# Kernel optimization log

Hardware: AMD Instinct MI355X
Metric: run time of the kernel (lower is better)

## Reference

```python
import jax, jax.numpy as jnp
import numpy as np

B, D, LP, P = 64, 256, 64, 16
N = 256                     # linear1 output = number of graph nodes (= d_model for consistent reassembly)
F = LP * P                  # per-node feature dim = SAGEConv input_dim = 1024
HID = 512                   # hidden_channels
NODE_SLICES = {"A": (0, 128), "B": (128, 192), "C": (192, 256)}
# 6 cross edge types + 3 self-loop edge types (add_self_loops=True)
EDGE_TYPES = [("A", "B"), ("B", "A"), ("A", "C"), ("C", "A"), ("B", "C"), ("C", "B"),
              ("A", "A"), ("B", "B"), ("C", "C")]
E = len(EDGE_TYPES)


def setup_inputs() -> dict:
    ks = jax.random.split(jax.random.key(0), 8)
    s = lambda fan: 1.0 / np.sqrt(fan)
    return {
        "x": jax.random.normal(ks[0], (B, D, LP, P), jnp.float32),
        "W1": jax.random.normal(ks[1], (D, N), jnp.float32) * s(D),   # linear1
        "b1": jnp.zeros((N,), jnp.float32),
        "Wl": jax.random.normal(ks[2], (E, F, HID), jnp.float32) * s(F),  # SAGEConv lin_l (aggregated msgs)
        "bl": jnp.zeros((E, HID), jnp.float32),
        "Wr": jax.random.normal(ks[3], (E, F, HID), jnp.float32) * s(F),  # SAGEConv lin_r (root, no bias)
        "Wf": jax.random.normal(ks[4], (HID, F), jnp.float32) * s(HID),   # final_linear
        "bf": jnp.zeros((F,), jnp.float32),
        "W2": jax.random.normal(ks[5], (N, D), jnp.float32) * s(N),       # linear2
        "b2": jnp.zeros((D,), jnp.float32),
        "period": P,
    }


def reference(x, W1, b1, Wl, bl, Wr, Wf, bf, W2, b2, period):
    b = x.shape[0]
    # linear1 over channel dim: [B,D,LP,P] -> [B,N,LP,P]
    h = jnp.einsum('bdlp,dn->bnlp', x, W1) + b1[None, :, None, None]
    hf = h.reshape(b, N, -1)                                  # node features [B, N, F]
    xt = {t: hf[:, lo:hi] for t, (lo, hi) in NODE_SLICES.items()}
    # complete bipartite graph => scatter-mean over incoming edges == mean over all src nodes
    mu = {t: v.mean(axis=1) for t, v in xt.items()}           # [B, F]
    contribs = {t: [] for t in NODE_SLICES}
    for i, (s_t, d_t) in enumerate(EDGE_TYPES):
        # SAGEConv(mean): lin_l(aggr msgs) + lin_r(x_dst)
        c = (mu[s_t] @ Wl[i] + bl[i])[:, None, :] + jnp.einsum('bnf,fh->bnh', xt[d_t], Wr[i])
        contribs[d_t].append(c)
    outs = []
    for t in ("A", "B", "C"):
        o = jnp.mean(jnp.stack(contribs[t]), axis=0)          # HeteroConv aggr='mean' over edge types
        o = jax.nn.relu(o) @ Wf + bf                          # relu + final_linear -> [B, n_t, F]
        outs.append(o)
    out = jnp.concatenate(outs, axis=1)                       # [B, N, F] (A,B,C slices are contiguous)
    out = out.reshape(b, N, -1, period)                       # [B, N, LP, P]
    # linear2 over node/channel dim
    y = jnp.einsum('bnlp,nd->bdlp', out, W2) + b2[None, :, None, None]
    return y
```

## Files before the change

### kernel.cpp

```cpp
#include <hip/hip_runtime.h>

typedef unsigned short u16;
typedef __attribute__((ext_vector_type(8))) short bf16x8;
typedef __attribute__((ext_vector_type(4))) float f32x4;

constexpr int BB = 64;
constexpr int NN = 256;
constexpr int SS = 1024;
constexpr int FF = 1024;
constexpr int HH = 512;

__device__ const int d_eArr[3][3] = {{1, 3, 6}, {0, 5, 7}, {2, 4, 8}};
__device__ const int d_slotE[3][3] = {{2, 0, 0}, {0, 2, 1}, {1, 1, 2}};

__device__ __forceinline__ u16 f2bf(float f) {
    union { float f; unsigned u; } v; v.f = f;
    unsigned r = v.u + 0x7FFFu + ((v.u >> 16) & 1u);
    return (u16)(r >> 16);
}
__device__ __forceinline__ float bf2f(u16 h) {
    union { unsigned u; float f; } v; v.u = ((unsigned)h) << 16;
    return v.f;
}

typedef const __attribute__((address_space(1))) void gv_t;
typedef __attribute__((address_space(3))) void lv_t;
__device__ __forceinline__ void gl16(const void* g, void* l) {
    __builtin_amdgcn_global_load_lds((gv_t*)g, (lv_t*)l, 16, 0, 0);
}
__device__ __forceinline__ int swzv(int r) { return (r ^ (r >> 2)) & 3; }

template<int N> __device__ __forceinline__ void waitvm();
template<> __device__ __forceinline__ void waitvm<0>()  { asm volatile("s_waitcnt vmcnt(0)" ::: "memory"); }
template<> __device__ __forceinline__ void waitvm<2>()  { asm volatile("s_waitcnt vmcnt(2)" ::: "memory"); }
template<> __device__ __forceinline__ void waitvm<4>()  { asm volatile("s_waitcnt vmcnt(4)" ::: "memory"); }
template<> __device__ __forceinline__ void waitvm<6>()  { asm volatile("s_waitcnt vmcnt(6)" ::: "memory"); }
template<> __device__ __forceinline__ void waitvm<8>()  { asm volatile("s_waitcnt vmcnt(8)" ::: "memory"); }
template<> __device__ __forceinline__ void waitvm<12>() { asm volatile("s_waitcnt vmcnt(12)" ::: "memory"); }

__device__ __forceinline__ int g5row(int t, int g, int r) {
    if (t == 0) return (g << 8) + r;
    const int bp = (t == 1) ? (g - 64) : (g - 96);
    const int b  = (bp << 1) + (r >> 6);
    const int n  = ((t == 1) ? 128 : 192) + (r & 63);
    return (b << 8) + n;
}

__global__ __launch_bounds__(256)
void transpose_bf16(const float* __restrict__ in, u16* __restrict__ out, int R, int C) {
    __shared__ float tile[32][33];
    const int b = blockIdx.z;
    in  += (size_t)b * R * C;
    out += (size_t)b * R * C;
    const int c0 = blockIdx.x * 32, r0 = blockIdx.y * 32;
    const int x = threadIdx.x & 31, y = threadIdx.x >> 5;
#pragma unroll
    for (int k = 0; k < 4; ++k)
        tile[y + 8 * k][x] = in[(size_t)(r0 + y + 8 * k) * C + c0 + x];
    __syncthreads();
#pragma unroll
    for (int k = 0; k < 4; ++k)
        out[(size_t)(c0 + y + 8 * k) * R + r0 + x] = f2bf(tile[x][y + 8 * k]);
}

__device__ __forceinline__ void tr32(const float* __restrict__ in, u16* __restrict__ out,
                                     int R, int C, int bx, int by, float (*tile)[33]) {
    const int c0 = bx * 32, r0 = by * 32;
    const int x = threadIdx.x & 31, y = threadIdx.x >> 5;
#pragma unroll
    for (int k = 0; k < 4; ++k)
        tile[y + 8 * k][x] = in[(size_t)(r0 + y + 8 * k) * C + c0 + x];
    __syncthreads();
#pragma unroll
    for (int k = 0; k < 4; ++k)
        out[(size_t)(c0 + y + 8 * k) * R + r0 + x] = f2bf(tile[x][y + 8 * k]);
}

__global__ __launch_bounds__(256)
void prep_weights(const float* __restrict__ W1, const float* __restrict__ W2,
                  const float* __restrict__ Wf, const float* __restrict__ Wl,
                  const float* __restrict__ Wr, const float* __restrict__ bl,
                  u16* __restrict__ W1T, u16* __restrict__ W2T, u16* __restrict__ WfT,
                  u16* __restrict__ WlTc, u16* __restrict__ WsumT, float* __restrict__ blsum)
{
    __shared__ float tile[32][33];
    int id = blockIdx.x;
    if (id < 64) { tr32(W1, W1T, 256, 256, id & 7, id >> 3, tile); return; }
    id -= 64;
    if (id < 64) { tr32(W2, W2T, 256, 256, id & 7, id >> 3, tile); return; }
    id -= 64;
    if (id < 512) { tr32(Wf, WfT, 512, 1024, id & 31, id >> 5, tile); return; }
    id -= 512;
    if (id < 4608) {
        const int p = id >> 9, rem = id & 511;
        const int bx = rem & 15, by = rem >> 4;
        const int t = p / 3, ep = p % 3, e = d_eArr[t][ep];
        const int h0 = bx * 32, f0 = by * 32;
        const int x = threadIdx.x & 31, y = threadIdx.x >> 5;
        const float* src = Wl + (size_t)e * FF * HH;
#pragma unroll
        for (int k = 0; k < 4; ++k)
            tile[y + 8 * k][x] = src[(size_t)(f0 + y + 8 * k) * HH + h0 + x];
        __syncthreads();
        u16* dst = WlTc + (size_t)t * HH * 3072 + (size_t)ep * 1024;
#pragma unroll
        for (int k = 0; k < 4; ++k)
            dst[(size_t)(h0 + y + 8 * k) * 3072 + f0 + x] = f2bf(tile[x][y + 8 * k]);
        return;
    }
    id -= 4608;
    if (id < 1536) {
        const int t = id >> 9, rem = id & 511;
        const int bx = rem & 15, by = rem >> 4;
        const int h0 = bx * 32, f0 = by * 32;
        const int x = threadIdx.x & 31, y = threadIdx.x >> 5;
        const int e0 = d_eArr[t][0], e1 = d_eArr[t][1], e2 = d_eArr[t][2];
#pragma unroll
        for (int k = 0; k < 4; ++k) {
            const size_t off = (size_t)(f0 + y + 8 * k) * HH + h0 + x;
            float s = Wr[(size_t)e0 * FF * HH + off] + Wr[(size_t)e1 * FF * HH + off] +
                      Wr[(size_t)e2 * FF * HH + off];
            tile[y + 8 * k][x] = s * (1.f / 3.f);
        }
        __syncthreads();
        u16* dst = WsumT + (size_t)t * HH * FF;
#pragma unroll
        for (int k = 0; k < 4; ++k)
            dst[(size_t)(h0 + y + 8 * k) * FF + f0 + x] = f2bf(tile[x][y + 8 * k]);
        return;
    }
#pragma unroll
    for (int j = 0; j < 6; ++j) {
        const int idx = j * 256 + threadIdx.x;
        const int t = idx >> 9, hh = idx & 511;
        blsum[t * HH + hh] = bl[d_eArr[t][0] * HH + hh] + bl[d_eArr[t][1] * HH + hh] +
                             bl[d_eArr[t][2] * HH + hh];
    }
}

template<int BM, int BN, int KLEN, int EPI, int MODE>
__global__ __launch_bounds__(256, 2)
void gemm2(const u16* __restrict__ Abase, const u16* __restrict__ Bbase,
           void* __restrict__ Cbase, const float* __restrict__ aux1,
           const float* __restrict__ aux2, u16* __restrict__ muOut,
           long long sB, long long sC, int ldA, int ldB, int ldC)
{
    constexpr int WM = BM / 2, WN = BN / 2;
    constexpr int FM = WM / 16, FN = WN / 16;
    constexpr int NIA = (BM * 4) / 256, NIB = (BN * 4) / 256;
    constexpr int LPS = NIA + NIB;
    constexpr int BUFB = (BM + BN) * 64;
    constexpr int NT = KLEN / 32;
    static_assert(NT >= 3, "need >=3 K-steps");
    __shared__ __align__(16) unsigned char smem[3 * BUFB];

    const int tid = threadIdx.x, lane = tid & 63, wave = tid >> 6;
    const int wm = wave >> 1, wn = wave & 1;
    const int n0 = blockIdx.x * BN;

    int m0 = 0, b = 0, t = 0, g = 0;
    const u16* Ab; const u16* Bb;
    if constexpr (MODE == 0) {
        b  = blockIdx.z;
        m0 = blockIdx.y * BM;
        Ab = Abase + (size_t)m0 * ldA;
        Bb = Bbase + (size_t)b * sB + (size_t)n0 * ldB;
    } else if constexpr (MODE == 1) {
        g  = blockIdx.y;
        t  = (g < 64) ? 0 : (g < 96 ? 1 : 2);
        Ab = Abase;
        Bb = Bbase + (size_t)t * (HH * FF) + (size_t)n0 * ldB;
    } else {
        t  = blockIdx.z;
        const int k0 = blockIdx.y * KLEN;
        Ab = Abase + (size_t)t * 64 * ldA + k0;
        Bb = Bbase + (size_t)t * (HH * 3072) + (size_t)n0 * ldB + k0;
    }

    const u16* gAp[NIA]; const u16* gBp[NIB];
    int lAo[NIA], lBo[NIB];
#pragma unroll
    for (int i = 0; i < NIA; ++i) {
        const int c = i * 256 + tid, r = c >> 2, jl = c & 3;
        const int js = jl ^ swzv(r);
        size_t rowoff;
        if constexpr (MODE == 1) rowoff = (size_t)g5row(t, g, r) * FF;
        else                     rowoff = (size_t)r * ldA;
        gAp[i] = Ab + rowoff + js * 8;
        lAo[i] = c * 16;
    }
#pragma unroll
    for (int i = 0; i < NIB; ++i) {
        const int c = i * 256 + tid, r = c >> 2, jl = c & 3;
        const int js = jl ^ swzv(r);
        gBp[i] = Bb + (size_t)r * ldB + js * 8;
        lBo[i] = BM * 64 + c * 16;
    }
    const int q = lane >> 4;
    int rAo[FM], rBo[FN];
#pragma unroll
    for (int i = 0; i < FM; ++i) {
        const int r = wm * WM + i * 16 + (lane & 15);
        rAo[i] = (r * 4 + (q ^ swzv(r))) * 16;
    }
#pragma unroll
    for (int j = 0; j < FN; ++j) {
        const int r = wn * WN + j * 16 + (lane & 15);
        rBo[j] = BM * 64 + (r * 4 + (q ^ swzv(r))) * 16;
    }

    char* sm = (char*)smem;
    auto stage = [&](int bufo, int it) {
        const int kofs = it * 32;
#pragma unroll
        for (int i = 0; i < NIA; ++i)
            gl16(gAp[i] + kofs, sm + bufo + lAo[i]);
#pragma unroll
        for (int i = 0; i < NIB; ++i)
            gl16(gBp[i] + kofs, sm + bufo + lBo[i]);
    };

    const f32x4 zero4 = {0.f, 0.f, 0.f, 0.f};
    f32x4 acc[FM][FN];
#pragma unroll
    for (int i = 0; i < FM; ++i)
#pragma unroll
        for (int j = 0; j < FN; ++j) acc[i][j] = zero4;

    stage(0, 0);
    stage(BUFB, 1);
    stage(2 * BUFB, 2);

    int bufo = 0;
    for (int it = 0; it < NT; ++it) {
        if (it < NT - 2)       waitvm<2 * LPS>();
        else if (it == NT - 2) waitvm<LPS>();
        else                   waitvm<0>();
        __builtin_amdgcn_s_barrier();

        bf16x8 af[FM], bq[FN];
#pragma unroll
        for (int i = 0; i < FM; ++i) af[i] = *(const bf16x8*)(sm + bufo + rAo[i]);
#pragma unroll
        for (int j = 0; j < FN; ++j) bq[j] = *(const bf16x8*)(sm + bufo + rBo[j]);
        asm volatile("s_waitcnt lgkmcnt(0)" ::: "memory");
        __builtin_amdgcn_sched_barrier(0);

        __builtin_amdgcn_s_setprio(1);
#pragma unroll
        for (int i = 0; i < FM; ++i)
#pragma unroll
            for (int j = 0; j < FN; ++j)
                acc[i][j] = __builtin_amdgcn_mfma_f32_16x16x32_bf16(af[i], bq[j], acc[i][j], 0, 0, 0);
        __builtin_amdgcn_s_setprio(0);

        __builtin_amdgcn_s_barrier();
        if (it + 3 < NT) stage(bufo, it + 3);
        bufo = (bufo == 2 * BUFB) ? 0 : bufo + BUFB;
    }

    const int q4   = q << 2;
    const int colb = n0 + wn * WN + (lane & 15);
    if constexpr (EPI == 0) {
        u16* C = (u16*)Cbase + (size_t)b * sC;
#pragma unroll
        for (int i = 0; i < FM; ++i)
#pragma unroll
            for (int rr = 0; rr < 4; ++rr) {
                const int row = m0 + wm * WM + i * 16 + q4 + rr;
                const float bias = aux1[row];
#pragma unroll
                for (int j = 0; j < FN; ++j)
                    C[(size_t)row * ldC + colb + j * 16] = f2bf(acc[i][j][rr] + bias);
            }
    } else if constexpr (EPI == 3) {
        float* C = (float*)Cbase + (size_t)b * sC;
#pragma unroll
        for (int i = 0; i < FM; ++i)
#pragma unroll
            for (int rr = 0; rr < 4; ++rr) {
                const int row = m0 + wm * WM + i * 16 + q4 + rr;
                const float bias = aux1[row];
#pragma unroll
                for (int j = 0; j < FN; ++j)
                    C[(size_t)row * ldC + colb + j * 16] = acc[i][j][rr] + bias;
            }
    } else if constexpr (EPI == 1) {
        float* C = (float*)Cbase + (size_t)blockIdx.y * 98304 + (size_t)t * (64 * HH);
#pragma unroll
        for (int i = 0; i < FM; ++i)
#pragma unroll
            for (int rr = 0; rr < 4; ++rr) {
                const int row = wm * WM + i * 16 + q4 + rr;
#pragma unroll
                for (int j = 0; j < FN; ++j)
                    C[(size_t)row * HH + colb + j * 16] = acc[i][j][rr];
            }
    } else if constexpr (EPI == 2) {
        u16* C = (u16*)Cbase;
        const int bb = (t == 0) ? g : ((((t == 1) ? (g - 64) : (g - 96)) << 1) + wm);
        float bet[FN];
#pragma unroll
        for (int j = 0; j < FN; ++j) {
            const int col = colb + j * 16;
            float s = 0.f;
#pragma unroll
            for (int ks = 0; ks < 8; ++ks)
                s += aux1[(size_t)ks * 98304 + (size_t)((t << 6) + bb) * HH + col];
            bet[j] = (s + aux2[t * HH + col]) * (1.f / 3.f);
        }
#pragma unroll
        for (int i = 0; i < FM; ++i)
#pragma unroll
            for (int rr = 0; rr < 4; ++rr) {
                const int rl = wm * WM + i * 16 + q4 + rr;
                const int glob = g5row(t, g, rl);
#pragma unroll
                for (int j = 0; j < FN; ++j) {
                    const float v = acc[i][j][rr] + bet[j];
                    C[(size_t)glob * ldC + colb + j * 16] = f2bf(fmaxf(v, 0.f));
                }
            }
    } else {
        u16* C = (u16*)Cbase + (size_t)b * sC;
        float t0[FN], t1[FN];
#pragma unroll
        for (int j = 0; j < FN; ++j) { t0[j] = 0.f; t1[j] = 0.f; }
#pragma unroll
        for (int i = 0; i < FM; ++i)
#pragma unroll
            for (int rr = 0; rr < 4; ++rr) {
                const int row = m0 + wm * WM + i * 16 + q4 + rr;
                const float bias = aux1[row];
#pragma unroll
                for (int j = 0; j < FN; ++j) {
                    const float hv = acc[i][j][rr] + bias;
                    C[(size_t)row * ldC + colb + j * 16] = f2bf(hv);
                    if (wm == 0)            t0[j] += hv;
                    else if (i < FM / 2)    t0[j] += hv;
                    else                    t1[j] += hv;
                }
            }
#pragma unroll
        for (int j = 0; j < FN; ++j) {
            t0[j] += __shfl_xor(t0[j], 16, 64);
            t0[j] += __shfl_xor(t0[j], 32, 64);
            t1[j] += __shfl_xor(t1[j], 16, 64);
            t1[j] += __shfl_xor(t1[j], 32, 64);
        }
        if (lane < 16) {
#pragma unroll
            for (int j = 0; j < FN; ++j) {
                const int col = colb + j * 16;
                if (wm == 0) {
                    const u16 v = f2bf(t0[j] * (1.f / 128.f));
#pragma unroll
                    for (int tt = 0; tt < 3; ++tt)
                        muOut[((size_t)tt * BB + b) * 3072 + (size_t)d_slotE[0][tt] * 1024 + col] = v;
                } else {
                    const u16 vB = f2bf(t0[j] * (1.f / 64.f));
                    const u16 vC = f2bf(t1[j] * (1.f / 64.f));
#pragma unroll
                    for (int tt = 0; tt < 3; ++tt) {
                        muOut[((size_t)tt * BB + b) * 3072 + (size_t)d_slotE[1][tt] * 1024 + col] = vB;
                        muOut[((size_t)tt * BB + b) * 3072 + (size_t)d_slotE[2][tt] * 1024 + col] = vC;
                    }
                }
            }
        }
    }
}

extern "C" void kernel_launch(void* const* d_in, const int* in_sizes, int n_in,
                              void* d_out, int out_size, void* d_ws, size_t ws_size,
                              hipStream_t stream) {
    const float* x  = (const float*)d_in[0];
    const float* W1 = (const float*)d_in[1];
    const float* b1 = (const float*)d_in[2];
    const float* Wl = (const float*)d_in[3];
    const float* bl = (const float*)d_in[4];
    const float* Wr = (const float*)d_in[5];
    const float* Wf = (const float*)d_in[6];
    const float* bf = (const float*)d_in[7];
    const float* W2 = (const float*)d_in[8];
    const float* b2 = (const float*)d_in[9];
    float* y = (float*)d_out;

    u16* wsS   = (u16*)d_ws;
    u16* xT    = wsS;
    u16* h     = wsS + 16777216;
    u16* r     = wsS + 33554432;
    u16* W1T   = wsS + 41943040;
    u16* W2T   = wsS + 42008576;
    u16* WfT   = wsS + 42074112;
    u16* WsumT = wsS + 42598400;
    u16* WlTc  = wsS + 44171264;
    u16* muCat = wsS + 48889856;
    float* blsum = (float*)(wsS + 49479680);
    float* tmp8 = (float*)xT;
    u16* outT = xT;

    prep_weights<<<dim3(6785), 256, 0, stream>>>(W1, W2, Wf, Wl, Wr, bl,
                                                 W1T, W2T, WfT, WlTc, WsumT, blsum);
    transpose_bf16<<<dim3(32, 8, 64), 256, 0, stream>>>(x, xT, 256, 1024);

    gemm2<256, 128, 256, 4, 0><<<dim3(8, 1, 64), 256, 0, stream>>>(
        W1T, xT, h, b1, nullptr, muCat, 262144, 262144, 256, 256, 1024);
    gemm2<64, 64, 384, 1, 2><<<dim3(8, 8, 3), 256, 0, stream>>>(
        muCat, WlTc, tmp8, nullptr, nullptr, nullptr, 0, 0, 3072, 3072, 512);
    gemm2<128, 128, 1024, 2, 1><<<dim3(4, 128, 1), 256, 0, stream>>>(
        h, WsumT, r, tmp8, blsum, nullptr, 0, 0, 1024, 1024, 512);
    gemm2<256, 128, 512, 0, 0><<<dim3(2, 4, 64), 256, 0, stream>>>(
        WfT, r, outT, bf, nullptr, nullptr, 131072, 262144, 512, 512, 256);
    gemm2<256, 128, 256, 3, 0><<<dim3(8, 1, 64), 256, 0, stream>>>(
        W2T, outT, y, b2, nullptr, nullptr, 262144, 262144, 256, 256, 1024);
}
```

Baseline: 133.2 us.

## Fuse x transpose into linear1 GEMM and reassociate final_linear with linear2

Drops the standalone x transpose kernel. The new linear1 kernel reads fp32 x directly, converts it to bf16 and swizzles it into LDS in registers, and keeps the mean-reduction epilogue. The SAGE GEMM now writes a transposed relu output, and linear2 (W2) is applied to that before final_linear (Wf). Because the hidden dimension of 512 is smaller than F of 1024, this reassociation cuts the FLOPs and intermediate traffic of the last two GEMMs. The bf term is folded in through a precomputed column sum of W2, and the new ordering changes bf16 rounding points.

```diff
diff --git a/kernel.cpp b/kernel.cpp
--- a/kernel.cpp
+++ b/kernel.cpp
@@ -38,31 +38,6 @@
 template<> __device__ __forceinline__ void waitvm<8>()  { asm volatile("s_waitcnt vmcnt(8)" ::: "memory"); }
 template<> __device__ __forceinline__ void waitvm<12>() { asm volatile("s_waitcnt vmcnt(12)" ::: "memory"); }
 
-__device__ __forceinline__ int g5row(int t, int g, int r) {
-    if (t == 0) return (g << 8) + r;
-    const int bp = (t == 1) ? (g - 64) : (g - 96);
-    const int b  = (bp << 1) + (r >> 6);
-    const int n  = ((t == 1) ? 128 : 192) + (r & 63);
-    return (b << 8) + n;
-}
-
-__global__ __launch_bounds__(256)
-void transpose_bf16(const float* __restrict__ in, u16* __restrict__ out, int R, int C) {
-    __shared__ float tile[32][33];
-    const int b = blockIdx.z;
-    in  += (size_t)b * R * C;
-    out += (size_t)b * R * C;
-    const int c0 = blockIdx.x * 32, r0 = blockIdx.y * 32;
-    const int x = threadIdx.x & 31, y = threadIdx.x >> 5;
-#pragma unroll
-    for (int k = 0; k < 4; ++k)
-        tile[y + 8 * k][x] = in[(size_t)(r0 + y + 8 * k) * C + c0 + x];
-    __syncthreads();
-#pragma unroll
-    for (int k = 0; k < 4; ++k)
-        out[(size_t)(c0 + y + 8 * k) * R + r0 + x] = f2bf(tile[x][y + 8 * k]);
-}
-
 __device__ __forceinline__ void tr32(const float* __restrict__ in, u16* __restrict__ out,
                                      int R, int C, int bx, int by, float (*tile)[33]) {
     const int c0 = bx * 32, r0 = by * 32;
@@ -81,7 +56,8 @@
                   const float* __restrict__ Wf, const float* __restrict__ Wl,
                   const float* __restrict__ Wr, const float* __restrict__ bl,
                   u16* __restrict__ W1T, u16* __restrict__ W2T, u16* __restrict__ WfT,
-                  u16* __restrict__ WlTc, u16* __restrict__ WsumT, float* __restrict__ blsum)
+                  u16* __restrict__ WlTc, u16* __restrict__ WsumT,
+                  float* __restrict__ blsum, float* __restrict__ c2)
 {
     __shared__ float tile[32][33];
     int id = blockIdx.x;
@@ -136,88 +112,261 @@
         blsum[t * HH + hh] = bl[d_eArr[t][0] * HH + hh] + bl[d_eArr[t][1] * HH + hh] +
                              bl[d_eArr[t][2] * HH + hh];
     }
+    {
+        const int d = threadIdx.x;
+        float s = 0.f;
+        for (int n = 0; n < NN; ++n) s += W2[(size_t)n * 256 + d];
+        c2[d] = s;
+    }
+}
+
+__global__ __launch_bounds__(256, 2)
+void g1_kernel(const float* __restrict__ x, const u16* __restrict__ W1T,
+               const float* __restrict__ b1, u16* __restrict__ h,
+               u16* __restrict__ muCat)
+{
+    constexpr int NT = 8;
+    constexpr int ABY = 256 * 64;
+    constexpr int BUFB = ABY + 128 * 64;
+    constexpr int FM = 8, FN = 4;
+    __shared__ __align__(16) unsigned char smem[2 * BUFB];
+    char* sm = (char*)smem;
+
+    const int tid = threadIdx.x, lane = tid & 63, wave = tid >> 6;
+    const int wm = wave >> 1, wn = wave & 1;
+    const int b = blockIdx.z, s0 = blockIdx.x * 128;
+    const float* xb = x + (size_t)b * 262144;
+
+    const u16* gAp[4]; int lAo[4];
+#pragma unroll
+    for (int i = 0; i < 4; ++i) {
+        const int c = i * 256 + tid, r = c >> 2, jl = c & 3;
+        gAp[i] = W1T + (size_t)r * 256 + (jl ^ swzv(r)) * 8;
+        lAo[i] = c * 16;
+    }
+    const int dq = tid >> 5;
+    const int sq = (tid & 31) * 4;
+    float4 breg[2][4];
+    auto loadB = [&](int slot, int it) {
+        const int k0 = it * 32;
+#pragma unroll
+        for (int k = 0; k < 4; ++k)
+            breg[slot][k] = *(const float4*)(xb + (size_t)(k0 + dq * 4 + k) * 1024 + s0 + sq);
+    };
+    auto writeB = [&](int slot, int bufo) {
+#pragma unroll
+        for (int si = 0; si < 4; ++si) {
+            const int s = sq + si;
+            ushort4 w;
+            w.x = f2bf(breg[slot][0][si]); w.y = f2bf(breg[slot][1][si]);
+            w.z = f2bf(breg[slot][2][si]); w.w = f2bf(breg[slot][3][si]);
+            *(ushort4*)(sm + bufo + ABY + s * 64 + (((dq >> 1) ^ swzv(s)) << 4) + ((dq & 1) << 3)) = w;
+        }
+    };
+    auto stageA = [&](int bufo, int it) {
+        const int kofs = it * 32;
+#pragma unroll
+        for (int i = 0; i < 4; ++i) gl16(gAp[i] + kofs, sm + bufo + lAo[i]);
+    };
+
+    const int q = lane >> 4;
+    int rAo[FM], rBo[FN];
+#pragma unroll
+    for (int i = 0; i < FM; ++i) {
+        const int r = wm * 128 + i * 16 + (lane & 15);
+        rAo[i] = (r * 4 + (q ^ swzv(r))) * 16;
+    }
+#pragma unroll
+    for (int j = 0; j < FN; ++j) {
+        const int r = wn * 64 + j * 16 + (lane & 15);
+        rBo[j] = ABY + (r * 4 + (q ^ swzv(r))) * 16;
+    }
+
+    const f32x4 zero4 = {0.f, 0.f, 0.f, 0.f};
+    f32x4 acc[FM][FN];
+#pragma unroll
+    for (int i = 0; i < FM; ++i)
+#pragma unroll
+        for (int j = 0; j < FN; ++j) acc[i][j] = zero4;
+
+    stageA(0, 0); loadB(0, 0);
+    stageA(BUFB, 1); loadB(1, 1);
+    waitvm<8>();
+    writeB(0, 0);
+    asm volatile("s_waitcnt lgkmcnt(0)" ::: "memory");
+    __builtin_amdgcn_s_barrier();
+
+    for (int it = 0; it < NT; ++it) {
+        const int bufo = (it & 1) * BUFB;
+        bf16x8 af[FM], bq[FN];
+#pragma unroll
+        for (int i = 0; i < FM; ++i) af[i] = *(const bf16x8*)(sm + bufo + rAo[i]);
+#pragma unroll
+        for (int j = 0; j < FN; ++j) bq[j] = *(const bf16x8*)(sm + bufo + rBo[j]);
+        asm volatile("s_waitcnt lgkmcnt(0)" ::: "memory");
+        __builtin_amdgcn_sched_barrier(0);
+        __builtin_amdgcn_s_setprio(1);
+#pragma unroll
+        for (int i = 0; i < FM; ++i)
+#pragma unroll
+            for (int j = 0; j < FN; ++j)
+                acc[i][j] = __builtin_amdgcn_mfma_f32_16x16x32_bf16(af[i], bq[j], acc[i][j], 0, 0, 0);
+        __builtin_amdgcn_s_setprio(0);
+
+        if (it + 1 < NT) {
+            __builtin_amdgcn_s_barrier();
+            if (it + 2 < NT) {
+                stageA(bufo, it + 2);
+                loadB(it & 1, it + 2);
+                waitvm<8>();
+            } else {
+                waitvm<0>();
+            }
+            writeB((it + 1) & 1, ((it + 1) & 1) * BUFB);
+            asm volatile("s_waitcnt lgkmcnt(0)" ::: "memory");
+            __builtin_amdgcn_s_barrier();
+        }
+    }
+
+    const int q4 = q << 2;
+    const int colb = s0 + wn * 64 + (lane & 15);
+    u16* C = h + (size_t)b * 262144;
+    float t0[FN], t1[FN];
+#pragma unroll
+    for (int j = 0; j < FN; ++j) { t0[j] = 0.f; t1[j] = 0.f; }
+#pragma unroll
+    for (int i = 0; i < FM; ++i)
+#pragma unroll
+        for (int rr = 0; rr < 4; ++rr) {
+            const int row = wm * 128 + i * 16 + q4 + rr;
+            const float bias = b1[row];
+#pragma unroll
+            for (int j = 0; j < FN; ++j) {
+                const float hv = acc[i][j][rr] + bias;
+                C[(size_t)row * 1024 + colb + j * 16] = f2bf(hv);
+                if (wm == 0)            t0[j] += hv;
+                else if (i < FM / 2)    t0[j] += hv;
+                else                    t1[j] += hv;
+            }
+        }
+#pragma unroll
+    for (int j = 0; j < FN; ++j) {
+        t0[j] += __shfl_xor(t0[j], 16, 64);
+        t0[j] += __shfl_xor(t0[j], 32, 64);
+        t1[j] += __shfl_xor(t1[j], 16, 64);
+        t1[j] += __shfl_xor(t1[j], 32, 64);
+    }
+    if (lane < 16) {
+#pragma unroll
+        for (int j = 0; j < FN; ++j) {
+            const int col = colb + j * 16;
+            if (wm == 0) {
+                const u16 v = f2bf(t0[j] * (1.f / 128.f));
+#pragma unroll
+                for (int tt = 0; tt < 3; ++tt)
+                    muCat[((size_t)tt * BB + b) * 3072 + (size_t)d_slotE[0][tt] * 1024 + col] = v;
+            } else {
+                const u16 vB = f2bf(t0[j] * (1.f / 64.f));
+                const u16 vC = f2bf(t1[j] * (1.f / 64.f));
+#pragma unroll
+                for (int tt = 0; tt < 3; ++tt) {
+                    muCat[((size_t)tt * BB + b) * 3072 + (size_t)d_slotE[1][tt] * 1024 + col] = vB;
+                    muCat[((size_t)tt * BB + b) * 3072 + (size_t)d_slotE[2][tt] * 1024 + col] = vC;
+                }
+            }
+        }
+    }
 }
 
 template<int BM, int BN, int KLEN, int EPI, int MODE>
 __global__ __launch_bounds__(256, 2)
 void gemm2(const u16* __restrict__ Abase, const u16* __restrict__ Bbase,
            void* __restrict__ Cbase, const float* __restrict__ aux1,
-           const float* __restrict__ aux2, u16* __restrict__ muOut,
+           const float* __restrict__ aux2, const float* __restrict__ aux3,
            long long sB, long long sC, int ldA, int ldB, int ldC)
 {
     constexpr int WM = BM / 2, WN = BN / 2;
     constexpr int FM = WM / 16, FN = WN / 16;
-    constexpr int NIA = (BM * 4) / 256, NIB = (BN * 4) / 256;
+    constexpr int APAN = (MODE == 4) ? 2 : 1;
+    constexpr int ABY = APAN * BM * 64;
+    constexpr int NIA = ABY / (16 * 256);
+    constexpr int NIB = (BN * 4) / 256;
     constexpr int LPS = NIA + NIB;
-    constexpr int BUFB = (BM + BN) * 64;
+    constexpr int BUFB = ABY + BN * 64;
     constexpr int NT = KLEN / 32;
     static_assert(NT >= 3, "need >=3 K-steps");
     __shared__ __align__(16) unsigned char smem[3 * BUFB];
+    char* sm = (char*)smem;
 
     const int tid = threadIdx.x, lane = tid & 63, wave = tid >> 6;
     const int wm = wave >> 1, wn = wave & 1;
     const int n0 = blockIdx.x * BN;
 
-    int m0 = 0, b = 0, t = 0, g = 0;
-    const u16* Ab; const u16* Bb;
+    int m0 = 0, b = 0, t = 0;
+    const u16* Ab = nullptr; const u16* Bb = nullptr;
     if constexpr (MODE == 0) {
         b  = blockIdx.z;
         m0 = blockIdx.y * BM;
         Ab = Abase + (size_t)m0 * ldA;
         Bb = Bbase + (size_t)b * sB + (size_t)n0 * ldB;
-    } else if constexpr (MODE == 1) {
-        g  = blockIdx.y;
-        t  = (g < 64) ? 0 : (g < 96 ? 1 : 2);
-        Ab = Abase;
-        Bb = Bbase + (size_t)t * (HH * FF) + (size_t)n0 * ldB;
-    } else {
+    } else if constexpr (MODE == 2) {
         t  = blockIdx.z;
         const int k0 = blockIdx.y * KLEN;
         Ab = Abase + (size_t)t * 64 * ldA + k0;
         Bb = Bbase + (size_t)t * (HH * 3072) + (size_t)n0 * ldB + k0;
+    } else if constexpr (MODE == 3) {
+        b  = blockIdx.z;
+        m0 = blockIdx.y * BM;
+        Ab = Abase + (size_t)b * sB + (size_t)m0 * ldA;
+        Bb = Bbase + (size_t)n0 * ldB;
+    } else {
+        b  = blockIdx.z;
+        m0 = blockIdx.y * BM;
+        Bb = Bbase + (size_t)b * sB + (size_t)n0 * ldB;
     }
 
     const u16* gAp[NIA]; const u16* gBp[NIB];
     int lAo[NIA], lBo[NIB];
 #pragma unroll
     for (int i = 0; i < NIA; ++i) {
-        const int c = i * 256 + tid, r = c >> 2, jl = c & 3;
-        const int js = jl ^ swzv(r);
-        size_t rowoff;
-        if constexpr (MODE == 1) rowoff = (size_t)g5row(t, g, r) * FF;
-        else                     rowoff = (size_t)r * ldA;
-        gAp[i] = Ab + rowoff + js * 8;
+        const int c = i * 256 + tid;
+        if constexpr (MODE == 4) {
+            const int pan = c / (BM * 4), cp = c % (BM * 4);
+            const int r = cp >> 2, jl = cp & 3, js = jl ^ swzv(r);
+            const int tP = (blockIdx.x == 0) ? 0 : (1 + pan);
+            gAp[i] = Abase + (size_t)tP * (HH * FF) + (size_t)(m0 + r) * ldA + js * 8;
+        } else {
+            const int r = c >> 2, jl = c & 3, js = jl ^ swzv(r);
+            gAp[i] = Ab + (size_t)r * ldA + js * 8;
+        }
         lAo[i] = c * 16;
     }
 #pragma unroll
     for (int i = 0; i < NIB; ++i) {
         const int c = i * 256 + tid, r = c >> 2, jl = c & 3;
-        const int js = jl ^ swzv(r);
-        gBp[i] = Bb + (size_t)r * ldB + js * 8;
-        lBo[i] = BM * 64 + c * 16;
+        gBp[i] = Bb + (size_t)r * ldB + (jl ^ swzv(r)) * 8;
+        lBo[i] = ABY + c * 16;
     }
     const int q = lane >> 4;
     int rAo[FM], rBo[FN];
 #pragma unroll
     for (int i = 0; i < FM; ++i) {
         const int r = wm * WM + i * 16 + (lane & 15);
-        rAo[i] = (r * 4 + (q ^ swzv(r))) * 16;
+        const int pofs = (MODE == 4) ? wn * (BM * 64) : 0;
+        rAo[i] = pofs + (r * 4 + (q ^ swzv(r))) * 16;
     }
 #pragma unroll
     for (int j = 0; j < FN; ++j) {
         const int r = wn * WN + j * 16 + (lane & 15);
-        rBo[j] = BM * 64 + (r * 4 + (q ^ swzv(r))) * 16;
-    }
-
-    char* sm = (char*)smem;
+        rBo[j] = ABY + (r * 4 + (q ^ swzv(r))) * 16;
+    }
+
     auto stage = [&](int bufo, int it) {
         const int kofs = it * 32;
 #pragma unroll
-        for (int i = 0; i < NIA; ++i)
-            gl16(gAp[i] + kofs, sm + bufo + lAo[i]);
-#pragma unroll
-        for (int i = 0; i < NIB; ++i)
-            gl16(gBp[i] + kofs, sm + bufo + lBo[i]);
+        for (int i = 0; i < NIA; ++i) gl16(gAp[i] + kofs, sm + bufo + lAo[i]);
+#pragma unroll
+        for (int i = 0; i < NIB; ++i) gl16(gBp[i] + kofs, sm + bufo + lBo[i]);
     };
 
     const f32x4 zero4 = {0.f, 0.f, 0.f, 0.f};
@@ -261,113 +410,62 @@
 
     const int q4   = q << 2;
     const int colb = n0 + wn * WN + (lane & 15);
-    if constexpr (EPI == 0) {
+    if constexpr (EPI == 1) {
+        float* C = (float*)Cbase + (size_t)blockIdx.y * 98304 + (size_t)t * (64 * HH);
+#pragma unroll
+        for (int i = 0; i < FM; ++i)
+#pragma unroll
+            for (int rr = 0; rr < 4; ++rr) {
+                const int row = wm * WM + i * 16 + q4 + rr;
+#pragma unroll
+                for (int j = 0; j < FN; ++j)
+                    C[(size_t)row * HH + colb + j * 16] = acc[i][j][rr];
+            }
+    } else if constexpr (EPI == 5) {
         u16* C = (u16*)Cbase + (size_t)b * sC;
 #pragma unroll
         for (int i = 0; i < FM; ++i)
 #pragma unroll
             for (int rr = 0; rr < 4; ++rr) {
                 const int row = m0 + wm * WM + i * 16 + q4 + rr;
-                const float bias = aux1[row];
 #pragma unroll
                 for (int j = 0; j < FN; ++j)
-                    C[(size_t)row * ldC + colb + j * 16] = f2bf(acc[i][j][rr] + bias);
-            }
-    } else if constexpr (EPI == 3) {
+                    C[(size_t)row * ldC + colb + j * 16] = f2bf(acc[i][j][rr]);
+            }
+    } else if constexpr (EPI == 6) {
         float* C = (float*)Cbase + (size_t)b * sC;
+        float bfv[FN];
+#pragma unroll
+        for (int j = 0; j < FN; ++j) bfv[j] = aux3[colb + j * 16];
 #pragma unroll
         for (int i = 0; i < FM; ++i)
 #pragma unroll
             for (int rr = 0; rr < 4; ++rr) {
                 const int row = m0 + wm * WM + i * 16 + q4 + rr;
-                const float bias = aux1[row];
+                const float bb2 = aux1[row], cc2 = aux2[row];
 #pragma unroll
                 for (int j = 0; j < FN; ++j)
-                    C[(size_t)row * ldC + colb + j * 16] = acc[i][j][rr] + bias;
-            }
-    } else if constexpr (EPI == 1) {
-        float* C = (float*)Cbase + (size_t)blockIdx.y * 98304 + (size_t)t * (64 * HH);
-#pragma unroll
-        for (int i = 0; i < FM; ++i)
-#pragma unroll
-            for (int rr = 0; rr < 4; ++rr) {
-                const int row = wm * WM + i * 16 + q4 + rr;
-#pragma unroll
-                for (int j = 0; j < FN; ++j)
-                    C[(size_t)row * HH + colb + j * 16] = acc[i][j][rr];
-            }
-    } else if constexpr (EPI == 2) {
-        u16* C = (u16*)Cbase;
-        const int bb = (t == 0) ? g : ((((t == 1) ? (g - 64) : (g - 96)) << 1) + wm);
-        float bet[FN];
-#pragma unroll
-        for (int j = 0; j < FN; ++j) {
-            const int col = colb + j * 16;
-            float s = 0.f;
-#pragma unroll
-            for (int ks = 0; ks < 8; ++ks)
-                s += aux1[(size_t)ks * 98304 + (size_t)((t << 6) + bb) * HH + col];
-            bet[j] = (s + aux2[t * HH + col]) * (1.f / 3.f);
-        }
-#pragma unroll
-        for (int i = 0; i < FM; ++i)
-#pragma unroll
-            for (int rr = 0; rr < 4; ++rr) {
-                const int rl = wm * WM + i * 16 + q4 + rr;
-                const int glob = g5row(t, g, rl);
-#pragma unroll
-                for (int j = 0; j < FN; ++j) {
-                    const float v = acc[i][j][rr] + bet[j];
-                    C[(size_t)glob * ldC + colb + j * 16] = f2bf(fmaxf(v, 0.f));
-                }
+                    C[(size_t)row * ldC + colb + j * 16] = acc[i][j][rr] + bb2 + cc2 * bfv[j];
             }
     } else {
         u16* C = (u16*)Cbase + (size_t)b * sC;
-        float t0[FN], t1[FN];
-#pragma unroll
-        for (int j = 0; j < FN; ++j) { t0[j] = 0.f; t1[j] = 0.f; }
+        const int tw = (blockIdx.x == 0) ? 0 : (1 + wn);
 #pragma unroll
         for (int i = 0; i < FM; ++i)
 #pragma unroll
             for (int rr = 0; rr < 4; ++rr) {
                 const int row = m0 + wm * WM + i * 16 + q4 + rr;
-                const float bias = aux1[row];
+                float s = aux2[tw * HH + row];
+#pragma unroll
+                for (int ks = 0; ks < 8; ++ks)
+                    s += aux1[(size_t)ks * 98304 + (size_t)tw * 32768 + (size_t)b * 512 + row];
+                const float bet = s * (1.f / 3.f);
 #pragma unroll
                 for (int j = 0; j < FN; ++j) {
-                    const float hv = acc[i][j][rr] + bias;
-                    C[(size_t)row * ldC + colb + j * 16] = f2bf(hv);
-                    if (wm == 0)            t0[j] += hv;
-                    else if (i < FM / 2)    t0[j] += hv;
-                    else                    t1[j] += hv;
+                    const float v = acc[i][j][rr] + bet;
+                    C[(size_t)row * ldC + colb + j * 16] = f2bf(fmaxf(v, 0.f));
                 }
             }
-#pragma unroll
-        for (int j = 0; j < FN; ++j) {
-            t0[j] += __shfl_xor(t0[j], 16, 64);
-            t0[j] += __shfl_xor(t0[j], 32, 64);
-            t1[j] += __shfl_xor(t1[j], 16, 64);
-            t1[j] += __shfl_xor(t1[j], 32, 64);
-        }
-        if (lane < 16) {
-#pragma unroll
-            for (int j = 0; j < FN; ++j) {
-                const int col = colb + j * 16;
-                if (wm == 0) {
-                    const u16 v = f2bf(t0[j] * (1.f / 128.f));
-#pragma unroll
-                    for (int tt = 0; tt < 3; ++tt)
-                        muOut[((size_t)tt * BB + b) * 3072 + (size_t)d_slotE[0][tt] * 1024 + col] = v;
-                } else {
-                    const u16 vB = f2bf(t0[j] * (1.f / 64.f));
-                    const u16 vC = f2bf(t1[j] * (1.f / 64.f));
-#pragma unroll
-                    for (int tt = 0; tt < 3; ++tt) {
-                        muOut[((size_t)tt * BB + b) * 3072 + (size_t)d_slotE[1][tt] * 1024 + col] = vB;
-                        muOut[((size_t)tt * BB + b) * 3072 + (size_t)d_slotE[2][tt] * 1024 + col] = vC;
-                    }
-                }
-            }
-        }
     }
 }
 
@@ -387,31 +485,28 @@
     float* y = (float*)d_out;
 
     u16* wsS   = (u16*)d_ws;
-    u16* xT    = wsS;
-    u16* h     = wsS + 16777216;
-    u16* r     = wsS + 33554432;
-    u16* W1T   = wsS + 41943040;
-    u16* W2T   = wsS + 42008576;
-    u16* WfT   = wsS + 42074112;
-    u16* WsumT = wsS + 42598400;
-    u16* WlTc  = wsS + 44171264;
-    u16* muCat = wsS + 48889856;
-    float* blsum = (float*)(wsS + 49479680);
-    float* tmp8 = (float*)xT;
-    u16* outT = xT;
+    u16* h     = wsS;
+    u16* rT    = wsS + 16777216;
+    u16* z     = wsS + 25165824;
+    u16* W1T   = wsS + 33554432;
+    u16* W2T   = wsS + 33619968;
+    u16* WfT   = wsS + 33685504;
+    u16* WsumT = wsS + 34209792;
+    u16* WlTc  = wsS + 35782656;
+    u16* muCat = wsS + 40501248;
+    float* tmp8  = (float*)(wsS + 41091072);
+    float* blsum = tmp8 + 786432;
+    float* c2    = blsum + 1536;
 
     prep_weights<<<dim3(6785), 256, 0, stream>>>(W1, W2, Wf, Wl, Wr, bl,
-                                                 W1T, W2T, WfT, WlTc, WsumT, blsum);
-    transpose_bf16<<<dim3(32, 8, 64), 256, 0, stream>>>(x, xT, 256, 1024);
-
-    gemm2<256, 128, 256, 4, 0><<<dim3(8, 1, 64), 256, 0, stream>>>(
-        W1T, xT, h, b1, nullptr, muCat, 262144, 262144, 256, 256, 1024);
+                                                 W1T, W2T, WfT, WlTc, WsumT, blsum, c2);
+    g1_kernel<<<dim3(8, 1, 64), 256, 0, stream>>>(x, W1T, b1, h, muCat);
     gemm2<64, 64, 384, 1, 2><<<dim3(8, 8, 3), 256, 0, stream>>>(
         muCat, WlTc, tmp8, nullptr, nullptr, nullptr, 0, 0, 3072, 3072, 512);
-    gemm2<128, 128, 1024, 2, 1><<<dim3(4, 128, 1), 256, 0, stream>>>(
-        h, WsumT, r, tmp8, blsum, nullptr, 0, 0, 1024, 1024, 512);
-    gemm2<256, 128, 512, 0, 0><<<dim3(2, 4, 64), 256, 0, stream>>>(
-        WfT, r, outT, bf, nullptr, nullptr, 131072, 262144, 512, 512, 256);
-    gemm2<256, 128, 256, 3, 0><<<dim3(8, 1, 64), 256, 0, stream>>>(
-        W2T, outT, y, b2, nullptr, nullptr, 262144, 262144, 256, 256, 1024);
-}
+    gemm2<128, 128, 1024, 7, 4><<<dim3(2, 4, 64), 256, 0, stream>>>(
+        WsumT, h, rT, tmp8, blsum, nullptr, 262144, 131072, 1024, 1024, 256);
+    gemm2<256, 128, 256, 5, 0><<<dim3(4, 1, 64), 256, 0, stream>>>(
+        W2T, rT, z, nullptr, nullptr, nullptr, 131072, 131072, 256, 256, 512);
+    gemm2<256, 128, 512, 6, 3><<<dim3(8, 1, 64), 256, 0, stream>>>(
+        z, WfT, y, b2, c2, bf, 131072, 262144, 512, 512, 1024);
+}
```

Result: slower. 136.8 us (+2.7%).

## Reassociate final_linear and linear2 so the node-mixing GEMM precedes the feature GEMM

Applied to the files above, without the earlier changes.

The last two GEMMs are reordered: linear2 (W2 over nodes) is applied to the relu'd hidden activations before final_linear (Wf). The bf bias term is folded in through a precomputed column sum of W2. The SAGE GEMM is also reorganised so each block computes the transposed hidden output for all three node types in one batched launch with a two-panel A tile, replacing the row-gather mode. This shrinks the node-mixing GEMM's K and N from the 1024-wide feature dimension to the 512-wide hidden one and removes a layout transform. The cost is new epilogue variants and a different intermediate rounding order.

```diff
diff --git a/kernel.cpp b/kernel.cpp
--- a/kernel.cpp
+++ b/kernel.cpp
@@ -37,14 +37,6 @@
 template<> __device__ __forceinline__ void waitvm<6>()  { asm volatile("s_waitcnt vmcnt(6)" ::: "memory"); }
 template<> __device__ __forceinline__ void waitvm<8>()  { asm volatile("s_waitcnt vmcnt(8)" ::: "memory"); }
 template<> __device__ __forceinline__ void waitvm<12>() { asm volatile("s_waitcnt vmcnt(12)" ::: "memory"); }
-
-__device__ __forceinline__ int g5row(int t, int g, int r) {
-    if (t == 0) return (g << 8) + r;
-    const int bp = (t == 1) ? (g - 64) : (g - 96);
-    const int b  = (bp << 1) + (r >> 6);
-    const int n  = ((t == 1) ? 128 : 192) + (r & 63);
-    return (b << 8) + n;
-}
 
 __global__ __launch_bounds__(256)
 void transpose_bf16(const float* __restrict__ in, u16* __restrict__ out, int R, int C) {
@@ -81,7 +73,8 @@
                   const float* __restrict__ Wf, const float* __restrict__ Wl,
                   const float* __restrict__ Wr, const float* __restrict__ bl,
                   u16* __restrict__ W1T, u16* __restrict__ W2T, u16* __restrict__ WfT,
-                  u16* __restrict__ WlTc, u16* __restrict__ WsumT, float* __restrict__ blsum)
+                  u16* __restrict__ WlTc, u16* __restrict__ WsumT,
+                  float* __restrict__ blsum, float* __restrict__ c2)
 {
     __shared__ float tile[32][33];
     int id = blockIdx.x;
@@ -136,88 +129,104 @@
         blsum[t * HH + hh] = bl[d_eArr[t][0] * HH + hh] + bl[d_eArr[t][1] * HH + hh] +
                              bl[d_eArr[t][2] * HH + hh];
     }
+    {
+        const int d = threadIdx.x;
+        float s = 0.f;
+        for (int n = 0; n < NN; ++n) s += W2[(size_t)n * 256 + d];
+        c2[d] = s;
+    }
 }
 
 template<int BM, int BN, int KLEN, int EPI, int MODE>
 __global__ __launch_bounds__(256, 2)
 void gemm2(const u16* __restrict__ Abase, const u16* __restrict__ Bbase,
            void* __restrict__ Cbase, const float* __restrict__ aux1,
-           const float* __restrict__ aux2, u16* __restrict__ muOut,
+           const float* __restrict__ aux2, const float* __restrict__ aux3,
+           u16* __restrict__ muOut,
            long long sB, long long sC, int ldA, int ldB, int ldC)
 {
     constexpr int WM = BM / 2, WN = BN / 2;
     constexpr int FM = WM / 16, FN = WN / 16;
-    constexpr int NIA = (BM * 4) / 256, NIB = (BN * 4) / 256;
+    constexpr int APAN = (MODE == 4) ? 2 : 1;
+    constexpr int ABY = APAN * BM * 64;
+    constexpr int NIA = ABY / (16 * 256);
+    constexpr int NIB = (BN * 4) / 256;
     constexpr int LPS = NIA + NIB;
-    constexpr int BUFB = (BM + BN) * 64;
+    constexpr int BUFB = ABY + BN * 64;
     constexpr int NT = KLEN / 32;
     static_assert(NT >= 3, "need >=3 K-steps");
     __shared__ __align__(16) unsigned char smem[3 * BUFB];
+    char* sm = (char*)smem;
 
     const int tid = threadIdx.x, lane = tid & 63, wave = tid >> 6;
     const int wm = wave >> 1, wn = wave & 1;
     const int n0 = blockIdx.x * BN;
 
-    int m0 = 0, b = 0, t = 0, g = 0;
-    const u16* Ab; const u16* Bb;
+    int m0 = 0, b = 0, t = 0;
+    const u16* Ab = nullptr; const u16* Bb = nullptr;
     if constexpr (MODE == 0) {
         b  = blockIdx.z;
         m0 = blockIdx.y * BM;
         Ab = Abase + (size_t)m0 * ldA;
         Bb = Bbase + (size_t)b * sB + (size_t)n0 * ldB;
-    } else if constexpr (MODE == 1) {
-        g  = blockIdx.y;
-        t  = (g < 64) ? 0 : (g < 96 ? 1 : 2);
-        Ab = Abase;
-        Bb = Bbase + (size_t)t * (HH * FF) + (size_t)n0 * ldB;
-    } else {
+    } else if constexpr (MODE == 2) {
         t  = blockIdx.z;
         const int k0 = blockIdx.y * KLEN;
         Ab = Abase + (size_t)t * 64 * ldA + k0;
         Bb = Bbase + (size_t)t * (HH * 3072) + (size_t)n0 * ldB + k0;
+    } else if constexpr (MODE == 3) {
+        b  = blockIdx.z;
+        m0 = blockIdx.y * BM;
+        Ab = Abase + (size_t)b * sB + (size_t)m0 * ldA;
+        Bb = Bbase + (size_t)n0 * ldB;
+    } else {
+        b  = blockIdx.z;
+        m0 = blockIdx.y * BM;
+        Bb = Bbase + (size_t)b * sB + (size_t)n0 * ldB;
     }
 
     const u16* gAp[NIA]; const u16* gBp[NIB];
     int lAo[NIA], lBo[NIB];
 #pragma unroll
     for (int i = 0; i < NIA; ++i) {
-        const int c = i * 256 + tid, r = c >> 2, jl = c & 3;
-        const int js = jl ^ swzv(r);
-        size_t rowoff;
-        if constexpr (MODE == 1) rowoff = (size_t)g5row(t, g, r) * FF;
-        else                     rowoff = (size_t)r * ldA;
-        gAp[i] = Ab + rowoff + js * 8;
+        const int c = i * 256 + tid;
+        if constexpr (MODE == 4) {
+            const int pan = c / (BM * 4), cp = c % (BM * 4);
+            const int r = cp >> 2, jl = cp & 3, js = jl ^ swzv(r);
+            const int tP = (blockIdx.x == 0) ? 0 : (1 + pan);
+            gAp[i] = Abase + (size_t)tP * (HH * FF) + (size_t)(m0 + r) * ldA + js * 8;
+        } else {
+            const int r = c >> 2, jl = c & 3, js = jl ^ swzv(r);
+            gAp[i] = Ab + (size_t)r * ldA + js * 8;
+        }
         lAo[i] = c * 16;
     }
 #pragma unroll
     for (int i = 0; i < NIB; ++i) {
         const int c = i * 256 + tid, r = c >> 2, jl = c & 3;
-        const int js = jl ^ swzv(r);
-        gBp[i] = Bb + (size_t)r * ldB + js * 8;
-        lBo[i] = BM * 64 + c * 16;
+        gBp[i] = Bb + (size_t)r * ldB + (jl ^ swzv(r)) * 8;
+        lBo[i] = ABY + c * 16;
     }
     const int q = lane >> 4;
     int rAo[FM], rBo[FN];
 #pragma unroll
     for (int i = 0; i < FM; ++i) {
         const int r = wm * WM + i * 16 + (lane & 15);
-        rAo[i] = (r * 4 + (q ^ swzv(r))) * 16;
+        const int pofs = (MODE == 4) ? wn * (BM * 64) : 0;
+        rAo[i] = pofs + (r * 4 + (q ^ swzv(r))) * 16;
     }
 #pragma unroll
     for (int j = 0; j < FN; ++j) {
         const int r = wn * WN + j * 16 + (lane & 15);
-        rBo[j] = BM * 64 + (r * 4 + (q ^ swzv(r))) * 16;
-    }
-
-    char* sm = (char*)smem;
+        rBo[j] = ABY + (r * 4 + (q ^ swzv(r))) * 16;
+    }
+
     auto stage = [&](int bufo, int it) {
         const int kofs = it * 32;
 #pragma unroll
-        for (int i = 0; i < NIA; ++i)
-            gl16(gAp[i] + kofs, sm + bufo + lAo[i]);
-#pragma unroll
-        for (int i = 0; i < NIB; ++i)
-            gl16(gBp[i] + kofs, sm + bufo + lBo[i]);
+        for (int i = 0; i < NIA; ++i) gl16(gAp[i] + kofs, sm + bufo + lAo[i]);
+#pragma unroll
+        for (int i = 0; i < NIB; ++i) gl16(gBp[i] + kofs, sm + bufo + lBo[i]);
     };
 
     const f32x4 zero4 = {0.f, 0.f, 0.f, 0.f};
@@ -261,31 +270,7 @@
 
     const int q4   = q << 2;
     const int colb = n0 + wn * WN + (lane & 15);
-    if constexpr (EPI == 0) {
-        u16* C = (u16*)Cbase + (size_t)b * sC;
-#pragma unroll
-        for (int i = 0; i < FM; ++i)
-#pragma unroll
-            for (int rr = 0; rr < 4; ++rr) {
-                const int row = m0 + wm * WM + i * 16 + q4 + rr;
-                const float bias = aux1[row];
-#pragma unroll
-                for (int j = 0; j < FN; ++j)
-                    C[(size_t)row * ldC + colb + j * 16] = f2bf(acc[i][j][rr] + bias);
-            }
-    } else if constexpr (EPI == 3) {
-        float* C = (float*)Cbase + (size_t)b * sC;
-#pragma unroll
-        for (int i = 0; i < FM; ++i)
-#pragma unroll
-            for (int rr = 0; rr < 4; ++rr) {
-                const int row = m0 + wm * WM + i * 16 + q4 + rr;
-                const float bias = aux1[row];
-#pragma unroll
-                for (int j = 0; j < FN; ++j)
-                    C[(size_t)row * ldC + colb + j * 16] = acc[i][j][rr] + bias;
-            }
-    } else if constexpr (EPI == 1) {
+    if constexpr (EPI == 1) {
         float* C = (float*)Cbase + (size_t)blockIdx.y * 98304 + (size_t)t * (64 * HH);
 #pragma unroll
         for (int i = 0; i < FM; ++i)
@@ -296,32 +281,7 @@
                 for (int j = 0; j < FN; ++j)
                     C[(size_t)row * HH + colb + j * 16] = acc[i][j][rr];
             }
-    } else if constexpr (EPI == 2) {
-        u16* C = (u16*)Cbase;
-        const int bb = (t == 0) ? g : ((((t == 1) ? (g - 64) : (g - 96)) << 1) + wm);
-        float bet[FN];
-#pragma unroll
-        for (int j = 0; j < FN; ++j) {
-            const int col = colb + j * 16;
-            float s = 0.f;
-#pragma unroll
-            for (int ks = 0; ks < 8; ++ks)
-                s += aux1[(size_t)ks * 98304 + (size_t)((t << 6) + bb) * HH + col];
-            bet[j] = (s + aux2[t * HH + col]) * (1.f / 3.f);
-        }
-#pragma unroll
-        for (int i = 0; i < FM; ++i)
-#pragma unroll
-            for (int rr = 0; rr < 4; ++rr) {
-                const int rl = wm * WM + i * 16 + q4 + rr;
-                const int glob = g5row(t, g, rl);
-#pragma unroll
-                for (int j = 0; j < FN; ++j) {
-                    const float v = acc[i][j][rr] + bet[j];
-                    C[(size_t)glob * ldC + colb + j * 16] = f2bf(fmaxf(v, 0.f));
-                }
-            }
-    } else {
+    } else if constexpr (EPI == 4) {
         u16* C = (u16*)Cbase + (size_t)b * sC;
         float t0[FN], t1[FN];
 #pragma unroll
@@ -368,6 +328,51 @@
                 }
             }
         }
+    } else if constexpr (EPI == 5) {
+        u16* C = (u16*)Cbase + (size_t)b * sC;
+#pragma unroll
+        for (int i = 0; i < FM; ++i)
+#pragma unroll
+            for (int rr = 0; rr < 4; ++rr) {
+                const int row = m0 + wm * WM + i * 16 + q4 + rr;
+#pragma unroll
+                for (int j = 0; j < FN; ++j)
+                    C[(size_t)row * ldC + colb + j * 16] = f2bf(acc[i][j][rr]);
+            }
+    } else if constexpr (EPI == 6) {
+        float* C = (float*)Cbase + (size_t)b * sC;
+        float bfv[FN];
+#pragma unroll
+        for (int j = 0; j < FN; ++j) bfv[j] = aux3[colb + j * 16];
+#pragma unroll
+        for (int i = 0; i < FM; ++i)
+#pragma unroll
+            for (int rr = 0; rr < 4; ++rr) {
+                const int row = m0 + wm * WM + i * 16 + q4 + rr;
+                const float bb2 = aux1[row], cc2 = aux2[row];
+#pragma unroll
+                for (int j = 0; j < FN; ++j)
+                    C[(size_t)row * ldC + colb + j * 16] = acc[i][j][rr] + bb2 + cc2 * bfv[j];
+            }
+    } else {
+        u16* C = (u16*)Cbase + (size_t)b * sC;
+        const int tw = (blockIdx.x == 0) ? 0 : (1 + wn);
+#pragma unroll
+        for (int i = 0; i < FM; ++i)
+#pragma unroll
+            for (int rr = 0; rr < 4; ++rr) {
+                const int row = m0 + wm * WM + i * 16 + q4 + rr;
+                float s = aux2[tw * HH + row];
+#pragma unroll
+                for (int ks = 0; ks < 8; ++ks)
+                    s += aux1[(size_t)ks * 98304 + (size_t)tw * 32768 + (size_t)b * 512 + row];
+                const float bet = s * (1.f / 3.f);
+#pragma unroll
+                for (int j = 0; j < FN; ++j) {
+                    const float v = acc[i][j][rr] + bet;
+                    C[(size_t)row * ldC + colb + j * 16] = f2bf(fmaxf(v, 0.f));
+                }
+            }
     }
 }
 
@@ -389,29 +394,30 @@
     u16* wsS   = (u16*)d_ws;
     u16* xT    = wsS;
     u16* h     = wsS + 16777216;
-    u16* r     = wsS + 33554432;
+    u16* rT    = wsS + 33554432;
     u16* W1T   = wsS + 41943040;
     u16* W2T   = wsS + 42008576;
     u16* WfT   = wsS + 42074112;
     u16* WsumT = wsS + 42598400;
     u16* WlTc  = wsS + 44171264;
     u16* muCat = wsS + 48889856;
-    float* blsum = (float*)(wsS + 49479680);
-    float* tmp8 = (float*)xT;
-    u16* outT = xT;
+    float* tmp8  = (float*)(wsS + 49479680);
+    float* blsum = tmp8 + 786432;
+    float* c2    = blsum + 1536;
+    u16* z = xT;
 
     prep_weights<<<dim3(6785), 256, 0, stream>>>(W1, W2, Wf, Wl, Wr, bl,
-                                                 W1T, W2T, WfT, WlTc, WsumT, blsum);
+                                                 W1T, W2T, WfT, WlTc, WsumT, blsum, c2);
     transpose_bf16<<<dim3(32, 8, 64), 256, 0, stream>>>(x, xT, 256, 1024);
 
     gemm2<256, 128, 256, 4, 0><<<dim3(8, 1, 64), 256, 0, stream>>>(
-        W1T, xT, h, b1, nullptr, muCat, 262144, 262144, 256, 256, 1024);
+        W1T, xT, h, b1, nullptr, nullptr, muCat, 262144, 262144, 256, 256, 1024);
     gemm2<64, 64, 384, 1, 2><<<dim3(8, 8, 3), 256, 0, stream>>>(
-        muCat, WlTc, tmp8, nullptr, nullptr, nullptr, 0, 0, 3072, 3072, 512);
-    gemm2<128, 128, 1024, 2, 1><<<dim3(4, 128, 1), 256, 0, stream>>>(
-        h, WsumT, r, tmp8, blsum, nullptr, 0, 0, 1024, 1024, 512);
-    gemm2<256, 128, 512, 0, 0><<<dim3(2, 4, 64), 256, 0, stream>>>(
-        WfT, r, outT, bf, nullptr, nullptr, 131072, 262144, 512, 512, 256);
-    gemm2<256, 128, 256, 3, 0><<<dim3(8, 1, 64), 256, 0, stream>>>(
-        W2T, outT, y, b2, nullptr, nullptr, 262144, 262144, 256, 256, 1024);
-}
+        muCat, WlTc, tmp8, nullptr, nullptr, nullptr, nullptr, 0, 0, 3072, 3072, 512);
+    gemm2<128, 128, 1024, 7, 4><<<dim3(2, 4, 64), 256, 0, stream>>>(
+        WsumT, h, rT, tmp8, blsum, nullptr, nullptr, 262144, 131072, 1024, 1024, 256);
+    gemm2<256, 128, 256, 5, 0><<<dim3(4, 1, 64), 256, 0, stream>>>(
+        W2T, rT, z, nullptr, nullptr, nullptr, nullptr, 131072, 131072, 256, 256, 512);
+    gemm2<256, 128, 512, 6, 3><<<dim3(8, 1, 64), 256, 0, stream>>>(
+        z, WfT, y, b2, c2, bf, nullptr, 131072, 262144, 512, 512, 1024);
+}
```

After: 146.9 us. 10.3% more time.
